# Kernel tuning notes

Measured on AMD Instinct MI355X. Metric: run time of the kernel, lower is better.

## Reference

```python
import jax, jax.numpy as jnp
import numpy as np

IN_C, OUT_C, K, G, STRIDE = 16, 16, 3, 64, 1
B, H, W = 16, 512, 512


def setup_inputs() -> dict:
    key = jax.random.key(0)
    k1, k2, k3 = jax.random.split(key, 3)
    x = jax.random.normal(k1, (B, IN_C, H, W), dtype=jnp.float32)
    spectral_params = jax.random.normal(k2, (K * IN_C, K * OUT_C), dtype=jnp.float32)
    attn_w = jax.random.normal(k3, (G, IN_C), dtype=jnp.float32) * 0.1  # 1x1 conv weight
    attn_b = jnp.zeros((G,), dtype=jnp.float32)                          # 1x1 conv bias
    return {"x": x, "spectral_params": spectral_params, "attn_w": attn_w, "attn_b": attn_b}


def _group_map():
    # radial frequency index over the [K*IN_C, K*OUT_C] spectral grid
    gi = jnp.linspace(-0.5, 0.5, K * IN_C)
    gj = jnp.linspace(-0.5, 0.5, K * OUT_C)
    idx = jnp.sqrt(gi[:, None] ** 2 + gj[None, :] ** 2)
    thresholds = jnp.linspace(0.0, 0.5, G + 1)
    # bucket i satisfies thresholds[i] <= idx < thresholds[i+1]
    gid = jnp.searchsorted(thresholds, idx, side='right') - 1
    valid = (idx < 0.5) & (gid >= 0) & (gid < G)
    return jnp.where(valid, gid, 0), valid


def reference(x, spectral_params, attn_w, attn_b):
    b, c, h, w = x.shape
    gid, valid = _group_map()  # [KC, KO] int, [KC, KO] bool
    # attention gate: global avg pool -> 1x1 conv -> sigmoid  -> [b, G]
    pooled = x.mean(axis=(2, 3))                              # [b, c]
    pi = jax.nn.sigmoid(pooled @ attn_w.T + attn_b)           # [b, G]
    # group masks are disjoint radial bands, so the mixture collapses to a
    # per-element gather of the gate value (0 outside all bands)
    gate = jnp.where(valid[None], pi[:, gid], 0.0)            # [b, KC, KO]
    dyn = spectral_params[None] * gate                        # [b, KC, KO]
    # view(in, k, out, k).permute(2,0,1,3) -> [b, out, in, k, k]
    dyn = dyn.reshape(b, IN_C, K, OUT_C, K).transpose(0, 3, 1, 2, 4)
    kernel = dyn.reshape(b * OUT_C, IN_C, K, K)
    # per-sample dynamic conv as a single grouped conv (groups = batch)
    out = jax.lax.conv_general_dilated(
        x.reshape(1, b * c, h, w), kernel,
        window_strides=(STRIDE, STRIDE), padding='VALID',
        dimension_numbers=('NCHW', 'OIHW', 'NCHW'),
        feature_group_count=b)
    return out.reshape(b, OUT_C, out.shape[2], out.shape[3])
```

## Files before the change

### kernel.cpp

```cpp
#include <hip/hip_runtime.h>


#define BATCH 16
#define CH 16
#define HIN 512
#define WIN 512
#define HOUT 510
#define WOUT 510

typedef _Float16 half8 __attribute__((ext_vector_type(8)));
typedef float f32x4 __attribute__((ext_vector_type(4)));


__global__ __launch_bounds__(256) void transform_kernel(const float* __restrict__ x,
                                                        unsigned short* __restrict__ xt,
                                                        float* __restrict__ psum) {
    const int blk = blockIdx.x;
    const int b = blk >> 8, within = blk & 255;
    const int tid = threadIdx.x;
    const int p0 = (within * 256 + tid) * 4;
    const float* xb = x + ((size_t)b << 22);

    f32x4 v[16];
    float s[16];
#pragma unroll
    for (int c = 0; c < 16; ++c) {
        v[c] = __builtin_nontemporal_load((const f32x4*)(xb + ((size_t)c << 18) + p0));
        s[c] = (v[c][0] + v[c][1]) + (v[c][2] + v[c][3]);
    }

    union { _Float16 h[64]; uint4 q[8]; } u;
#pragma unroll
    for (int c = 0; c < 16; ++c) {
        u.h[0 * 16 + c] = (_Float16)v[c][0];
        u.h[1 * 16 + c] = (_Float16)v[c][1];
        u.h[2 * 16 + c] = (_Float16)v[c][2];
        u.h[3 * 16 + c] = (_Float16)v[c][3];
    }
    uint4* dst = (uint4*)(xt + ((size_t)((b << 18) + p0)) * 16);
#pragma unroll
    for (int k = 0; k < 8; ++k) dst[k] = u.q[k];

#pragma unroll
    for (int c = 0; c < 16; ++c) {
        float r = s[c];
        r += __shfl_xor(r, 1);  r += __shfl_xor(r, 2);  r += __shfl_xor(r, 4);
        r += __shfl_xor(r, 8);  r += __shfl_xor(r, 16); r += __shfl_xor(r, 32);
        s[c] = r;
    }
    if ((tid & 63) == 0) {
        float* ps = psum + (size_t)(b * 1024 + within * 4 + (tid >> 6)) * 16;
#pragma unroll
        for (int c = 0; c < 16; ++c) ps[c] = s[c];
    }
}

__global__ __launch_bounds__(256) void stage2_kernel(const float* __restrict__ psum,
                                                     const float* __restrict__ attn_w,
                                                     const float* __restrict__ attn_b,
                                                     const float* __restrict__ spectral,
                                                     unsigned short* __restrict__ wpack) {
    const int b = blockIdx.x, t = threadIdx.x;
    const int c = t & 15, m = t >> 4;
    float s = 0.f;
    for (int j = 0; j < 64; ++j) s += psum[((size_t)b * 1024 + m + j * 16) * 16 + c];
    __shared__ float red[256];
    __shared__ float pooled[16];
    __shared__ float pis[64];
    red[t] = s;
    __syncthreads();
    for (int off = 8; off; off >>= 1) {
        if (m < off) red[t] += red[t + off * 16];
        __syncthreads();
    }
    if (t < 16) pooled[t] = red[t] * (1.f / 262144.f);
    __syncthreads();
    if (t < 64) {
        float a = attn_b[t];
#pragma unroll
        for (int c2 = 0; c2 < 16; ++c2) a += pooled[c2] * attn_w[t * 16 + c2];
        pis[t] = 1.f / (1.f + expf(-a));
    }
    __syncthreads();
    for (int e = t; e < 320; e += 256) {
        const int c5 = e >> 6, lane = e & 63;
        const int o = lane & 15, g = lane >> 4;
        union { _Float16 h[8]; uint4 q; } u;
#pragma unroll
        for (int j = 0; j < 8; ++j) {
            const int kap = c5 * 32 + g * 8 + j;
            const int tp = kap >> 4, i = kap & 15;
            float wv = 0.f;
            if (tp < 9) {
                const int ki = tp / 3, kj = tp - ki * 3;
                const int r = i * 3 + ki, cc = o * 3 + kj;
                const float gi = -0.5f + (float)r * (1.f / 47.f);
                const float gj = -0.5f + (float)cc * (1.f / 47.f);
                const float d2 = gi * gi + gj * gj;
                if (d2 < 0.25f) {
                    int gid = (int)(sqrtf(d2) * 128.f);
                    gid = gid < 63 ? gid : 63;
                    wv = spectral[r * 48 + cc] * pis[gid];
                }
            }
            u.h[j] = (_Float16)wv;
        }
        *(uint4*)(wpack + ((size_t)(b * 5 + c5) * 64 + lane) * 8) = u.q;
    }
}

#define ROWP 16384
__global__ __launch_bounds__(512) void conv_mfma_kernel(const unsigned short* __restrict__ xt,
                                                        const unsigned short* __restrict__ wpack,
                                                        float* __restrict__ out) {
    const int b = blockIdx.y;
    const int y0 = blockIdx.x * 2;

    const int tid = threadIdx.x;
    const int lane = tid & 63, wv = tid >> 6;
    const int n = lane & 15, g = lane >> 4;
    const int cg = wv & 3, rw = wv >> 2;
    const int y = y0 + rw;

    __shared__ unsigned char lds[4 * ROWP];

    half8 wf[5];
    {
        const uint4* wp = (const uint4*)wpack + (size_t)b * 5 * 64 + lane;
#pragma unroll
        for (int c5 = 0; c5 < 5; ++c5) wf[c5] = __builtin_bit_cast(half8, wp[c5 * 64]);
    }

    {
        const uint4* xb = (const uint4*)xt + ((size_t)b << 19);
#pragma unroll
        for (int k = 0; k < 8; ++k) {
            const int e = tid + k * 512;
            const int rr = e >> 10, q = e & 1023;
            const uint4 v = xb[((size_t)(y0 + rr) << 10) + q];
            unsigned a = (unsigned)(e << 4);
            a ^= (a >> 3) & 0x30u;
            *(uint4*)(lds + a) = v;
        }
    }
    __syncthreads();

    unsigned q0[5], rb[5];
#pragma unroll
    for (int c5 = 0; c5 < 5; ++c5) {
        const int tp = 2 * c5 + (g >> 1);
        if (tp == 9) {
            q0[c5] = 0; rb[c5] = 0;
        } else {
            const int dy = tp / 3, dx = tp - dy * 3;
            q0[c5] = (unsigned)((cg * 128 + n + dx) * 32 + (g & 1) * 16);
            rb[c5] = (unsigned)((rw + dy) * ROWP);
        }
    }

    float* dst0 = out + ((size_t)(b * 16 + n) * HOUT + y) * WOUT + cg * 128 + g * 4;

#pragma unroll
    for (int tt = 0; tt < 8; ++tt) {
        half8 xf[5];
#pragma unroll
        for (int c5 = 0; c5 < 5; ++c5) {
            unsigned a = (q0[c5] + tt * 512u) & 16383u;
            a ^= (a >> 3) & 0x30u;
            xf[c5] = __builtin_bit_cast(half8, *(const uint4*)(lds + (rb[c5] + a)));
        }
        f32x4 acc = {0.f, 0.f, 0.f, 0.f};
#pragma unroll
        for (int c5 = 0; c5 < 5; ++c5)
            acc = __builtin_amdgcn_mfma_f32_16x16x32_f16(xf[c5], wf[c5], acc, 0, 0, 0);
        const int pb = cg * 128 + tt * 16 + g * 4;
        float* dst = dst0 + tt * 16;
        if (pb + 3 < WOUT) {
            ((float2*)dst)[0] = make_float2(acc[0], acc[1]);
            ((float2*)dst)[1] = make_float2(acc[2], acc[3]);
        } else {
#pragma unroll
            for (int r = 0; r < 4; ++r)
                if (pb + r < WOUT) dst[r] = acc[r];
        }
    }
}

#define TW 128
#define TH 8
#define XW 132

__global__ __launch_bounds__(256) void pool_kernel(const float* __restrict__ x,
                                                   float* __restrict__ pooled) {
    const int bc = blockIdx.x;
    const float4* src = (const float4*)(x + ((size_t)bc << 18));
    float s = 0.f;
    for (int e = threadIdx.x; e < (HIN * WIN / 4); e += 256) {
        float4 v = src[e];
        s += (v.x + v.y) + (v.z + v.w);
    }
    __shared__ float red[256];
    red[threadIdx.x] = s;
    __syncthreads();
    for (int off = 128; off > 0; off >>= 1) {
        if (threadIdx.x < off) red[threadIdx.x] += red[threadIdx.x + off];
        __syncthreads();
    }
    if (threadIdx.x == 0) pooled[bc] = red[0] * (1.0f / (HIN * WIN));
}

__global__ __launch_bounds__(256) void attn_kernel(const float* __restrict__ pooled,
                                                   const float* __restrict__ attn_w,
                                                   const float* __restrict__ attn_b,
                                                   float* __restrict__ pi) {
    int t = blockIdx.x * 256 + threadIdx.x;
    if (t >= BATCH * 64) return;
    int b = t >> 6, g = t & 63;
    float s = attn_b[g];
#pragma unroll
    for (int c = 0; c < CH; ++c) s += pooled[b * CH + c] * attn_w[g * CH + c];
    pi[t] = 1.0f / (1.0f + expf(-s));
}

__global__ __launch_bounds__(256) void weight_kernel(const float* __restrict__ spectral,
                                                     const float* __restrict__ pi,
                                                     float* __restrict__ wbuf) {
    int idx = blockIdx.x * 256 + threadIdx.x;
    if (idx >= BATCH * CH * CH * 12) return;
    int tap = idx % 12;
    int o = (idx / 12) % CH;
    int i = (idx / 192) % CH;
    int b = idx / 3072;
    float w = 0.f;
    if (tap < 9) {
        int ki = tap / 3, kj = tap % 3;
        int r = i * 3 + ki, c = o * 3 + kj;
        float gi = -0.5f + (float)r * (1.0f / 47.0f);
        float gj = -0.5f + (float)c * (1.0f / 47.0f);
        float d2 = gi * gi + gj * gj;
        if (d2 < 0.25f) {
            int gid = (int)(sqrtf(d2) * 128.0f);
            gid = gid < 63 ? gid : 63;
            w = spectral[r * 48 + c] * pi[b * 64 + gid];
        }
    }
    wbuf[idx] = w;
}

__global__ __launch_bounds__(256) void conv_kernel(const float* __restrict__ x,
                                                   const float* __restrict__ wbuf,
                                                   float* __restrict__ out) {
    const int b = blockIdx.y;
    const int tc = blockIdx.x & 3;
    const int tr = blockIdx.x >> 2;
    __shared__ float xs[10 * XW];
    __shared__ float ws[CH * CH * 12];
    {
        const float4* src = (const float4*)(wbuf + (size_t)b * (CH * CH * 12));
        float4* dst = (float4*)ws;
        for (int e = threadIdx.x; e < 768; e += 256) dst[e] = src[e];
    }
    const int r0 = tr * TH, c0 = tc * TW;
    const int px = (threadIdx.x & 31) * 4, py = threadIdx.x >> 5;
    float acc[16][4];
#pragma unroll
    for (int o = 0; o < 16; ++o)
#pragma unroll
        for (int p = 0; p < 4; ++p) acc[o][p] = 0.f;
    for (int i = 0; i < CH; ++i) {
        __syncthreads();
        const float* xsrc = x + (((size_t)b * CH + i) << 18);
        for (int e = threadIdx.x; e < 330; e += 256) {
            int rr = e / 33;
            int c4 = (e - rr * 33) * 4;
            int ir = r0 + rr, ic = c0 + c4;
            float4 v;
            if (ir < HIN && ic + 3 < WIN) {
                v = *(const float4*)(xsrc + ((size_t)ir << 9) + ic);
            } else {
                v.x = v.y = v.z = v.w = 0.f;
                if (ir < HIN) {
                    const float* row = xsrc + ((size_t)ir << 9);
                    if (ic + 0 < WIN) v.x = row[ic + 0];
                    if (ic + 1 < WIN) v.y = row[ic + 1];
                    if (ic + 2 < WIN) v.z = row[ic + 2];
                    if (ic + 3 < WIN) v.w = row[ic + 3];
                }
            }
            *(float4*)(xs + rr * XW + c4) = v;
        }
        __syncthreads();
        float xv[3][8];
#pragma unroll
        for (int kr = 0; kr < 3; ++kr) {
            float4 a = *(const float4*)(xs + (py + kr) * XW + px);
            float4 c = *(const float4*)(xs + (py + kr) * XW + px + 4);
            xv[kr][0] = a.x; xv[kr][1] = a.y; xv[kr][2] = a.z; xv[kr][3] = a.w;
            xv[kr][4] = c.x; xv[kr][5] = c.y; xv[kr][6] = c.z; xv[kr][7] = c.w;
        }
#pragma unroll
        for (int o = 0; o < 16; ++o) {
            const float* wrow = ws + (i * 16 + o) * 12;
            float4 w0 = *(const float4*)wrow;
            float4 w1 = *(const float4*)(wrow + 4);
            float w8 = wrow[8];
#pragma unroll
            for (int p = 0; p < 4; ++p) {
                float s = acc[o][p];
                s += xv[0][p + 0] * w0.x;
                s += xv[0][p + 1] * w0.y;
                s += xv[0][p + 2] * w0.z;
                s += xv[1][p + 0] * w0.w;
                s += xv[1][p + 1] * w1.x;
                s += xv[1][p + 2] * w1.y;
                s += xv[2][p + 0] * w1.z;
                s += xv[2][p + 1] * w1.w;
                s += xv[2][p + 2] * w8;
                acc[o][p] = s;
            }
        }
    }
    const int oy = r0 + py, ox = c0 + px;
    if (oy < HOUT) {
#pragma unroll
        for (int o = 0; o < 16; ++o) {
            float* orow = out + (((size_t)(b * 16 + o)) * HOUT + oy) * WOUT + ox;
            if (ox + 3 < WOUT) {
                ((float2*)orow)[0] = make_float2(acc[o][0], acc[o][1]);
                ((float2*)orow)[1] = make_float2(acc[o][2], acc[o][3]);
            } else {
#pragma unroll
                for (int p = 0; p < 4; ++p)
                    if (ox + p < WOUT) orow[p] = acc[o][p];
            }
        }
    }
}

extern "C" void kernel_launch(void* const* d_in, const int* in_sizes, int n_in,
                              void* d_out, int out_size, void* d_ws, size_t ws_size,
                              hipStream_t stream) {
    const float* x = (const float*)d_in[0];
    const float* spectral = (const float*)d_in[1];
    const float* attn_w = (const float*)d_in[2];
    const float* attn_b = (const float*)d_in[3];
    float* out = (float*)d_out;

    const size_t XT_BYTES = (size_t)16 * 512 * 512 * 16 * 2;
    const size_t PSUM_BYTES = (size_t)16 * 1024 * 16 * 4;
    const size_t WPACK_BYTES = (size_t)16 * 5 * 64 * 8 * 2;
    const size_t NEED = XT_BYTES + PSUM_BYTES + WPACK_BYTES;

    if (ws_size >= NEED) {
        unsigned short* xt = (unsigned short*)d_ws;
        float* psum = (float*)((char*)d_ws + XT_BYTES);
        unsigned short* wpack = (unsigned short*)((char*)d_ws + XT_BYTES + PSUM_BYTES);

        transform_kernel<<<dim3(4096), dim3(256), 0, stream>>>(x, xt, psum);
        stage2_kernel<<<dim3(16), dim3(256), 0, stream>>>(psum, attn_w, attn_b, spectral, wpack);
        conv_mfma_kernel<<<dim3(255, 16), dim3(512), 0, stream>>>(xt, wpack, out);
    } else {
        float* ws = (float*)d_ws;
        float* pooled = ws;
        float* pi = ws + 256;
        float* wbuf = ws + 1280;
        pool_kernel<<<dim3(BATCH * CH), dim3(256), 0, stream>>>(x, pooled);
        attn_kernel<<<dim3(4), dim3(256), 0, stream>>>(pooled, attn_w, attn_b, pi);
        weight_kernel<<<dim3((BATCH * CH * CH * 12 + 255) / 256), dim3(256), 0, stream>>>(spectral, pi, wbuf);
        conv_kernel<<<dim3(4 * 64, BATCH), dim3(256), 0, stream>>>(x, wbuf, out);
    }
}
```

Baseline: 199.2 us.

## Use global_load_lds for conv tile staging, packed fp16 convert, LDS block reduction

The conv kernel now stages input rows straight from global memory into LDS with global_load_lds, applying the same XOR swizzle on the source index, so the data no longer passes through registers. The transform kernel packs fp16 pairs with cvt_pkrtz, which rounds toward zero instead of to nearest. It also reduces the per-channel partial sums across the whole block through LDS, so psum gets one entry per block instead of one per wave and stage2 reads fewer values. The changes trade extra LDS use and a block barrier in the transform kernel for less register traffic and fewer global writes.

```diff
diff --git a/kernel.cpp b/kernel.cpp
--- a/kernel.cpp
+++ b/kernel.cpp
@@ -10,6 +10,7 @@
 
 typedef _Float16 half8 __attribute__((ext_vector_type(8)));
 typedef float f32x4 __attribute__((ext_vector_type(4)));
+typedef _Float16 half2v __attribute__((ext_vector_type(2)));
 
 
 __global__ __launch_bounds__(256) void transform_kernel(const float* __restrict__ x,
@@ -29,30 +30,28 @@
         s[c] = (v[c][0] + v[c][1]) + (v[c][2] + v[c][3]);
     }
 
-    union { _Float16 h[64]; uint4 q[8]; } u;
-#pragma unroll
-    for (int c = 0; c < 16; ++c) {
-        u.h[0 * 16 + c] = (_Float16)v[c][0];
-        u.h[1 * 16 + c] = (_Float16)v[c][1];
-        u.h[2 * 16 + c] = (_Float16)v[c][2];
-        u.h[3 * 16 + c] = (_Float16)v[c][3];
-    }
+    union { unsigned w[32]; uint4 q[8]; } u;
+#pragma unroll
+    for (int m = 0; m < 4; ++m)
+#pragma unroll
+        for (int jj = 0; jj < 8; ++jj)
+            u.w[m * 8 + jj] = __builtin_bit_cast(unsigned,
+                __builtin_amdgcn_cvt_pkrtz(v[2 * jj][m], v[2 * jj + 1][m]));
     uint4* dst = (uint4*)(xt + ((size_t)((b << 18) + p0)) * 16);
 #pragma unroll
     for (int k = 0; k < 8; ++k) dst[k] = u.q[k];
 
-#pragma unroll
-    for (int c = 0; c < 16; ++c) {
-        float r = s[c];
-        r += __shfl_xor(r, 1);  r += __shfl_xor(r, 2);  r += __shfl_xor(r, 4);
-        r += __shfl_xor(r, 8);  r += __shfl_xor(r, 16); r += __shfl_xor(r, 32);
-        s[c] = r;
-    }
-    if ((tid & 63) == 0) {
-        float* ps = psum + (size_t)(b * 1024 + within * 4 + (tid >> 6)) * 16;
-#pragma unroll
-        for (int c = 0; c < 16; ++c) ps[c] = s[c];
-    }
+    __shared__ float red[16 * 256];
+#pragma unroll
+    for (int c = 0; c < 16; ++c) red[c * 256 + tid] = s[c];
+    __syncthreads();
+    const int rc = tid >> 4, rp = tid & 15;
+    float s1 = 0.f;
+#pragma unroll
+    for (int j = 0; j < 16; ++j) s1 += red[rc * 256 + rp * 16 + j];
+    s1 += __shfl_xor(s1, 1); s1 += __shfl_xor(s1, 2);
+    s1 += __shfl_xor(s1, 4); s1 += __shfl_xor(s1, 8);
+    if (rp == 0) psum[(size_t)(b * 256 + within) * 16 + rc] = s1;
 }
 
 __global__ __launch_bounds__(256) void stage2_kernel(const float* __restrict__ psum,
@@ -63,7 +62,8 @@
     const int b = blockIdx.x, t = threadIdx.x;
     const int c = t & 15, m = t >> 4;
     float s = 0.f;
-    for (int j = 0; j < 64; ++j) s += psum[((size_t)b * 1024 + m + j * 16) * 16 + c];
+#pragma unroll
+    for (int j = 0; j < 16; ++j) s += psum[(size_t)(b * 256 + m * 16 + j) * 16 + c];
     __shared__ float red[256];
     __shared__ float pooled[16];
     __shared__ float pis[64];
@@ -122,7 +122,8 @@
     const int cg = wv & 3, rw = wv >> 2;
     const int y = y0 + rw;
 
-    __shared__ unsigned char lds[4 * ROWP];
+    __shared__ uint4 ldsbuf[4096];
+    unsigned char* ldsb = (unsigned char*)ldsbuf;
 
     half8 wf[5];
     {
@@ -135,12 +136,13 @@
         const uint4* xb = (const uint4*)xt + ((size_t)b << 19);
 #pragma unroll
         for (int k = 0; k < 8; ++k) {
-            const int e = tid + k * 512;
-            const int rr = e >> 10, q = e & 1023;
-            const uint4 v = xb[((size_t)(y0 + rr) << 10) + q];
-            unsigned a = (unsigned)(e << 4);
-            a ^= (a >> 3) & 0x30u;
-            *(uint4*)(lds + a) = v;
+            const int e = k * 512 + tid;
+            const int ep = e ^ ((e >> 3) & 3);
+            const int rr = ep >> 10, q = ep & 1023;
+            __builtin_amdgcn_global_load_lds(
+                (const __attribute__((address_space(1))) void*)(xb + (((size_t)(y0 + rr)) << 10) + q),
+                (__attribute__((address_space(3))) void*)(&ldsbuf[e]),
+                16, 0, 0);
         }
     }
     __syncthreads();
@@ -167,7 +169,7 @@
         for (int c5 = 0; c5 < 5; ++c5) {
             unsigned a = (q0[c5] + tt * 512u) & 16383u;
             a ^= (a >> 3) & 0x30u;
-            xf[c5] = __builtin_bit_cast(half8, *(const uint4*)(lds + (rb[c5] + a)));
+            xf[c5] = __builtin_bit_cast(half8, *(const uint4*)(ldsb + (rb[c5] + a)));
         }
         f32x4 acc = {0.f, 0.f, 0.f, 0.f};
 #pragma unroll
```

After: 184.4 us. -7.4%, faster.
